# Performance work log

Measured on AMD Instinct MI355X. Metric: run time of the kernel, lower is better.

Reference implementation:

```python
import jax, jax.numpy as jnp
import numpy as np

HIDDEN = 1024
HEADS = 16
HEAD_DIM = HIDDEN // HEADS


def setup_inputs() -> dict:
    key = jax.random.key(0)
    ks = jax.random.split(key, 9)
    B, S = 2, 2048
    std = 1.0 / np.sqrt(HIDDEN)
    inp = {
        'hidden_states': jax.random.normal(ks[0], (B, S, HIDDEN), dtype=jnp.float32),
        'attention_mask': jnp.ones((B, S), dtype=jnp.int32),
        'wq': jax.random.normal(ks[1], (HIDDEN, HIDDEN), dtype=jnp.float32) * std,
        'bq': jnp.zeros((HIDDEN,), dtype=jnp.float32),
        'wk': jax.random.normal(ks[2], (HIDDEN, HIDDEN), dtype=jnp.float32) * std,
        'bk': jnp.zeros((HIDDEN,), dtype=jnp.float32),
        'wv': jax.random.normal(ks[3], (HIDDEN, HIDDEN), dtype=jnp.float32) * std,
        'bv': jnp.zeros((HIDDEN,), dtype=jnp.float32),
        'wo': jax.random.normal(ks[4], (HIDDEN, HIDDEN), dtype=jnp.float32) * std,
        'bo': jnp.zeros((HIDDEN,), dtype=jnp.float32),
    }
    return inp


def reference(hidden_states, attention_mask, wq, bq, wk, bk, wv, bv, wo, bo):
    B, S, H = hidden_states.shape
    def heads(x):  # [B,S,H] -> [B,nh,S,hd]
        return x.reshape(B, S, HEADS, HEAD_DIM).transpose(0, 2, 1, 3)
    q = heads(hidden_states @ wq + bq)
    k = heads(hidden_states @ wk + bk)
    v = heads(hidden_states @ wv + bv)
    scores = jnp.einsum('bhqd,bhkd->bhqk', q, k) / np.sqrt(HEAD_DIM).astype(np.float32)
    causal = jnp.tril(jnp.ones((S, S), dtype=bool))  # True = keep
    keep = causal[None, None] & (attention_mask[:, None, None, :] != 0)
    scores = jnp.where(keep, scores, -jnp.inf)
    probs = jax.nn.softmax(scores, axis=-1)
    out = jnp.einsum('bhqk,bhkd->bhqd', probs, v)  # [B,nh,S,hd]
    out = out.transpose(0, 2, 1, 3).reshape(B, S, H)
    return out @ wo + bo
```

## Files before the change

kernel.cpp:

```cpp
#include <hip/hip_runtime.h>

#define HID   1024
#define SLEN  2048
#define NHEAD 16
#define HDIM  64
#define SC2L  0.18033688f

typedef unsigned short u16;
typedef _Float16 f16;
using bf16x8 = __attribute__((ext_vector_type(8))) short;
using f16x4  = __attribute__((ext_vector_type(4))) f16;
using f32x4  = __attribute__((ext_vector_type(4))) float;

typedef __attribute__((address_space(1))) void gvoid;
typedef __attribute__((address_space(3))) void lvoid;

__device__ __forceinline__ u16 f2bf(float f) {
  union { float f; unsigned u; } v; v.f = f;
  unsigned u = v.u;
  return (u16)((u + 0x7fffu + ((u >> 16) & 1u)) >> 16);
}

__device__ __forceinline__ void async_ld16(const u16* g, u16* l) {
  __builtin_amdgcn_global_load_lds((gvoid*)g, (lvoid*)l, 16, 0, 0);
}

__global__ __launch_bounds__(256) void prep_kernel(const float* __restrict__ x,
                                                   const float* __restrict__ wq,
                                                   const float* __restrict__ wk,
                                                   const float* __restrict__ wv,
                                                   const float* __restrict__ wo,
                                                   u16* __restrict__ xb,
                                                   u16* __restrict__ wt) {
  const int tid = threadIdx.x;
  if (blockIdx.z == 4) {
    const int bid = blockIdx.y * 32 + blockIdx.x;
#pragma unroll
    for (int it = 0; it < 4; ++it) {
      const int i = bid * 1024 + it * 256 + tid;
      float4 v = ((const float4*)x)[i];
      ushort4 o;
      o.x = f2bf(v.x); o.y = f2bf(v.y); o.z = f2bf(v.z); o.w = f2bf(v.w);
      ((ushort4*)xb)[i] = o;
    }
    return;
  }
  const float* src = (blockIdx.z == 0) ? wq : (blockIdx.z == 1) ? wk
                   : (blockIdx.z == 2) ? wv : wo;
  u16* dst = wt + (size_t)blockIdx.z * (HID * HID);
  __shared__ float tile[32][33];
  const int n0 = blockIdx.x * 32, k0 = blockIdx.y * 32;
  const int xx = tid & 31, yy = tid >> 5;
  for (int i = yy; i < 32; i += 8)
    tile[i][xx] = src[(size_t)(k0 + i) * HID + n0 + xx];
  __syncthreads();
  for (int i = yy; i < 32; i += 8)
    dst[(size_t)(n0 + i) * HID + k0 + xx] = f2bf(tile[xx][i]);
}

__global__ __launch_bounds__(256) void gemm_qkv_kernel(const u16* __restrict__ A,
                                                       const u16* __restrict__ Bt,
                                                       const float* __restrict__ bq,
                                                       const float* __restrict__ bk,
                                                       const float* __restrict__ bv,
                                                       u16* __restrict__ Qb,
                                                       u16* __restrict__ Kb,
                                                       u16* __restrict__ VTf) {
  __shared__ u16 smem[8192];
  u16* sA = smem;
  u16* sB = smem + 4096;
  const int tid  = threadIdx.x;
  const int wave = tid >> 6, lane = tid & 63;
  const int quad = lane >> 4, l16 = lane & 15;
  const int n0g = blockIdx.x * 128;
  const int region = blockIdx.x >> 3;
  const int colbase = (blockIdx.x & 7) * 128;
  const int m0 = blockIdx.y * 128;
  const int wm = (wave & 1) * 64, wn = (wave >> 1) * 64;

  f32x4 acc[4][4] = {};
  const int srow = lane >> 2;
  const int scol = (lane & 3) * 8;

  for (int kt = 0; kt < HID; kt += 32) {
    __syncthreads();
    for (int c = wave; c < 8; c += 4) {
      async_ld16(A  + (size_t)(m0  + c * 16 + srow) * HID + kt + scol, &sA[c * 512]);
      async_ld16(Bt + (size_t)(n0g + c * 16 + srow) * HID + kt + scol, &sB[c * 512]);
    }
    __syncthreads();

    bf16x8 af[4], bfr[4];
#pragma unroll
    for (int t = 0; t < 4; ++t) {
      af[t]  = *(const bf16x8*)&sA[(wm + t * 16 + l16) * 32 + quad * 8];
      bfr[t] = *(const bf16x8*)&sB[(wn + t * 16 + l16) * 32 + quad * 8];
    }
#pragma unroll
    for (int mt = 0; mt < 4; ++mt)
#pragma unroll
      for (int nt = 0; nt < 4; ++nt)
        acc[mt][nt] = __builtin_amdgcn_mfma_f32_16x16x32_bf16(af[mt], bfr[nt],
                                                              acc[mt][nt], 0, 0, 0);
  }

  const float* bias = (region == 0) ? bq : (region == 1) ? bk : bv;
  float bvv[4];
#pragma unroll
  for (int nt = 0; nt < 4; ++nt) bvv[nt] = bias[colbase + wn + nt * 16 + l16];

  if (region == 2) {
    const int bb = m0 >> 11;
    const int m0loc = m0 & 2047;
    const int h0 = colbase >> 6;
    u16* T = smem;
#pragma unroll
    for (int h2 = 0; h2 < 2; ++h2) {
      __syncthreads();
      if ((wave >> 1) == h2) {
#pragma unroll
        for (int mt = 0; mt < 4; ++mt)
#pragma unroll
          for (int nt = 0; nt < 4; ++nt)
#pragma unroll
            for (int r = 0; r < 4; ++r) {
              const int sl = (wave & 1) * 64 + mt * 16 + quad * 4 + r;
              const int dl = nt * 16 + l16;
              union { f16 h; u16 u; } cv;
              cv.h = (f16)(acc[mt][nt][r] + bvv[nt]);
              T[dl * 128 + (((sl >> 3) ^ l16) * 8) + (sl & 7)] = cv.u;
            }
      }
      __syncthreads();
      const int d = tid >> 2, sg = (tid & 3) * 4;
      u16* drow = VTf + (size_t)((bb * NHEAD + h0 + h2) * HDIM + d) * SLEN + m0loc;
#pragma unroll
      for (int cc = 0; cc < 4; ++cc) {
        const int cl = sg + cc;
        const int ph = cl ^ (d & 15);
        *(bf16x8*)(drow + cl * 8) = *(const bf16x8*)&T[d * 128 + ph * 8];
      }
    }
    return;
  }

  u16* C = (region == 0) ? Qb : Kb;
#pragma unroll
  for (int mt = 0; mt < 4; ++mt)
#pragma unroll
    for (int r = 0; r < 4; ++r) {
      const int row = m0 + wm + mt * 16 + quad * 4 + r;
#pragma unroll
      for (int nt = 0; nt < 4; ++nt) {
        const int col = colbase + wn + nt * 16 + l16;
        C[(size_t)row * HID + col] = f2bf(acc[mt][nt][r] + bvv[nt]);
      }
    }
}

__global__ __launch_bounds__(256) void gemm_o_kernel(const u16* __restrict__ A,
                                                     const u16* __restrict__ Bt,
                                                     const float* __restrict__ bias,
                                                     float* __restrict__ Cf) {
  __shared__ u16 sA[64 * 32];
  __shared__ u16 sB[128 * 32];
  const int tid  = threadIdx.x;
  const int wave = tid >> 6, lane = tid & 63;
  const int quad = lane >> 4, l16 = lane & 15;
  const int n0 = blockIdx.x * 128;
  const int m0 = blockIdx.y * 64;
  const int wn = wave * 32;

  f32x4 acc[4][2] = {};
  const int srow = lane >> 2;
  const int scol = (lane & 3) * 8;

  for (int kt = 0; kt < HID; kt += 32) {
    __syncthreads();
    for (int c = wave; c < 12; c += 4) {
      if (c < 4) async_ld16(A  + (size_t)(m0 + c * 16 + srow) * HID + kt + scol, &sA[c * 512]);
      else       async_ld16(Bt + (size_t)(n0 + (c - 4) * 16 + srow) * HID + kt + scol,
                            &sB[(c - 4) * 512]);
    }
    __syncthreads();

    bf16x8 af[4], bfr[2];
#pragma unroll
    for (int t = 0; t < 4; ++t)
      af[t] = *(const bf16x8*)&sA[(t * 16 + l16) * 32 + quad * 8];
#pragma unroll
    for (int t = 0; t < 2; ++t)
      bfr[t] = *(const bf16x8*)&sB[(wn + t * 16 + l16) * 32 + quad * 8];
#pragma unroll
    for (int mt = 0; mt < 4; ++mt)
#pragma unroll
      for (int nt = 0; nt < 2; ++nt)
        acc[mt][nt] = __builtin_amdgcn_mfma_f32_16x16x32_bf16(af[mt], bfr[nt],
                                                              acc[mt][nt], 0, 0, 0);
  }

  float bvv[2];
#pragma unroll
  for (int nt = 0; nt < 2; ++nt) bvv[nt] = bias[n0 + wn + nt * 16 + l16];
#pragma unroll
  for (int mt = 0; mt < 4; ++mt)
#pragma unroll
    for (int r = 0; r < 4; ++r) {
      const int row = m0 + mt * 16 + quad * 4 + r;
#pragma unroll
      for (int nt = 0; nt < 2; ++nt)
        Cf[(size_t)row * HID + n0 + wn + nt * 16 + l16] = acc[mt][nt][r] + bvv[nt];
    }
}

__global__ __launch_bounds__(256, 2) void flash_attn_kernel(const u16* __restrict__ Q,
                                                            const u16* __restrict__ K,
                                                            const u16* __restrict__ VT,
                                                            const int* __restrict__ mask,
                                                            u16* __restrict__ O) {
  const int xb = blockIdx.x, h = blockIdx.y, b = blockIdx.z;
  const int tid  = threadIdx.x;
  const int wave = tid >> 6, lane = tid & 63;
  const int quad = lane >> 4, l16 = lane & 15;

  __shared__ alignas(16) char smraw[35840];
  u16*   Ks  = (u16*)smraw;
  u16*   Vt  = (u16*)(smraw + 16384);
  float* Ob0 = (float*)smraw;
  float* Ob1 = (float*)(smraw + 16896);
  float* lb  = (float*)(smraw + 33792);

  const u16* Kh  = K  + (size_t)b * SLEN * HID + h * HDIM;
  const u16* Vth = VT + (size_t)((b * NHEAD + h) * HDIM) * SLEN;

  const int srow8 = lane >> 3;
  const int gch   = (lane & 7) ^ srow8;
  const int rx    = l16 & 7;

  for (int phase = 0; phase < 2; ++phase) {
    const int qt = phase ? (31 - xb) : xb;
    const int q0 = qt * 64;

    bf16x8 qb[4][2];
#pragma unroll
    for (int nt = 0; nt < 4; ++nt) {
      const u16* qp = Q + (size_t)(b * SLEN + q0 + nt * 16 + l16) * HID + h * HDIM + quad * 8;
      qb[nt][0] = *(const bf16x8*)qp;
      qb[nt][1] = *(const bf16x8*)(qp + 32);
    }

    f32x4 oacc[4][4] = {};
    float l_part[4] = {0.f, 0.f, 0.f, 0.f};

    {
      const int r0 = wave * 16 + srow8;
      async_ld16(Kh  + (size_t)r0 * HID + gch * 8,        Ks + wave * 1024);
      async_ld16(Kh  + (size_t)(r0 + 8) * HID + gch * 8,  Ks + wave * 1024 + 512);
      async_ld16(Vth + (size_t)r0 * SLEN + gch * 8,       Vt + wave * 1024);
      async_ld16(Vth + (size_t)(r0 + 8) * SLEN + gch * 8, Vt + wave * 1024 + 512);
    }
    __syncthreads();

    for (int j = 0; j <= qt; ++j) {
      const int buf = j & 1;
      u16* KsB = Ks + buf * 4096;
      u16* VtB = Vt + buf * 4096;

      if (j < qt) {
        const int nb = (buf ^ 1) * 4096;
        const int jn = (j + 1) * 64;
        const int r0 = wave * 16 + srow8;
        async_ld16(Kh  + (size_t)(jn + r0) * HID + gch * 8,       Ks + nb + wave * 1024);
        async_ld16(Kh  + (size_t)(jn + r0 + 8) * HID + gch * 8,   Ks + nb + wave * 1024 + 512);
        async_ld16(Vth + (size_t)r0 * SLEN + jn + gch * 8,        Vt + nb + wave * 1024);
        async_ld16(Vth + (size_t)(r0 + 8) * SLEN + jn + gch * 8,  Vt + nb + wave * 1024 + 512);
      }

      const int4 mi = *(const int4*)(mask + b * SLEN + j * 64 + wave * 16 + quad * 4);
      float map[4];
      map[0] = mi.x ? 0.f : -1e30f;  map[1] = mi.y ? 0.f : -1e30f;
      map[2] = mi.z ? 0.f : -1e30f;  map[3] = mi.w ? 0.f : -1e30f;

      const u16* kp = KsB + (wave * 16 + l16) * 64;
      const int ph0 = quad ^ rx;
      const bf16x8 ka0 = *(const bf16x8*)(kp + ph0 * 8);
      const bf16x8 ka1 = *(const bf16x8*)(kp + (ph0 ^ 4) * 8);

      float p[4][4];
#pragma unroll
      for (int nt = 0; nt < 4; ++nt) {
        f32x4 z = {0.f, 0.f, 0.f, 0.f};
        z = __builtin_amdgcn_mfma_f32_16x16x32_bf16(ka0, qb[nt][0], z, 0, 0, 0);
        z = __builtin_amdgcn_mfma_f32_16x16x32_bf16(ka1, qb[nt][1], z, 0, 0, 0);
#pragma unroll
        for (int r = 0; r < 4; ++r)
          p[nt][r] = exp2f(fmaf(z[r], SC2L, map[r]));
      }
      if (j == qt) {
#pragma unroll
        for (int nt = 0; nt < 4; ++nt)
#pragma unroll
          for (int r = 0; r < 4; ++r)
            if (wave * 16 + quad * 4 + r > nt * 16 + l16) p[nt][r] = 0.f;
      }

      f16x4 pb[4];
#pragma unroll
      for (int nt = 0; nt < 4; ++nt) {
        l_part[nt] += (p[nt][0] + p[nt][1]) + (p[nt][2] + p[nt][3]);
        pb[nt][0] = (f16)p[nt][0]; pb[nt][1] = (f16)p[nt][1];
        pb[nt][2] = (f16)p[nt][2]; pb[nt][3] = (f16)p[nt][3];
      }

      const int phv = (wave * 2 + (quad >> 1)) ^ rx;
      const int vsub = phv * 8 + (quad & 1) * 4;
#pragma unroll
      for (int dt = 0; dt < 4; ++dt) {
        const f16x4 va = *(const f16x4*)(VtB + (dt * 16 + l16) * 64 + vsub);
#pragma unroll
        for (int nt = 0; nt < 4; ++nt)
          oacc[dt][nt] = __builtin_amdgcn_mfma_f32_16x16x16f16(va, pb[nt], oacc[dt][nt], 0, 0, 0);
      }
      __syncthreads();
    }

#pragma unroll
    for (int nt = 0; nt < 4; ++nt) {
      l_part[nt] += __shfl_xor(l_part[nt], 16);
      l_part[nt] += __shfl_xor(l_part[nt], 32);
    }
    if (quad == 0)
#pragma unroll
      for (int nt = 0; nt < 4; ++nt) lb[wave * 64 + nt * 16 + l16] = l_part[nt];

    if ((wave & 1) == 0) {
      float* ob = (wave == 0) ? Ob0 : Ob1;
#pragma unroll
      for (int dt = 0; dt < 4; ++dt)
#pragma unroll
        for (int nt = 0; nt < 4; ++nt)
#pragma unroll
          for (int r = 0; r < 4; ++r)
            ob[(dt * 16 + quad * 4 + r) * 66 + nt * 16 + l16] = oacc[dt][nt][r];
    }
    __syncthreads();
    if (wave & 1) {
      float* ob = (wave == 1) ? Ob0 : Ob1;
#pragma unroll
      for (int dt = 0; dt < 4; ++dt)
#pragma unroll
        for (int nt = 0; nt < 4; ++nt)
#pragma unroll
          for (int r = 0; r < 4; ++r)
            ob[(dt * 16 + quad * 4 + r) * 66 + nt * 16 + l16] += oacc[dt][nt][r];
    }
    __syncthreads();

    {
      const int q  = tid >> 2;
      const int dc = tid & 3;
      const float l = lb[q] + lb[64 + q] + lb[128 + q] + lb[192 + q];
      const float inv = 1.f / l;
      u16 ob[16];
#pragma unroll
      for (int e = 0; e < 16; ++e) {
        const int d = dc * 16 + e;
        ob[e] = f2bf((Ob0[d * 66 + q] + Ob1[d * 66 + q]) * inv);
      }
      u16* op = O + (size_t)(b * SLEN + q0 + q) * HID + h * HDIM + dc * 16;
      *(bf16x8*)op       = *(bf16x8*)&ob[0];
      *(bf16x8*)(op + 8) = *(bf16x8*)&ob[8];
    }
    __syncthreads();
  }
}

extern "C" void kernel_launch(void* const* d_in, const int* in_sizes, int n_in,
                              void* d_out, int out_size, void* d_ws, size_t ws_size,
                              hipStream_t stream) {
  const float* x    = (const float*)d_in[0];
  const int*   mask = (const int*)d_in[1];
  const float* wq   = (const float*)d_in[2];
  const float* bq   = (const float*)d_in[3];
  const float* wk   = (const float*)d_in[4];
  const float* bk   = (const float*)d_in[5];
  const float* wv   = (const float*)d_in[6];
  const float* bv   = (const float*)d_in[7];
  const float* wo   = (const float*)d_in[8];
  const float* bo   = (const float*)d_in[9];
  float* out = (float*)d_out;

  char* ws = (char*)d_ws;
  u16* XBF = (u16*)(ws);
  u16* WT  = (u16*)(ws + (8u  << 20));
  u16* QBF = (u16*)(ws + (16u << 20));
  u16* KBF = (u16*)(ws + (24u << 20));
  u16* VTF = (u16*)(ws + (32u << 20));
  u16* ATT = (u16*)(ws);

  prep_kernel<<<dim3(32, 32, 5), 256, 0, stream>>>(x, wq, wk, wv, wo, XBF, WT);
  gemm_qkv_kernel<<<dim3(24, 32), 256, 0, stream>>>(XBF, WT, bq, bk, bv, QBF, KBF, VTF);
  flash_attn_kernel<<<dim3(16, NHEAD, 2), 256, 0, stream>>>(QBF, KBF, VTF, mask, ATT);
  gemm_o_kernel<<<dim3(8, 64), 256, 0, stream>>>(ATT, WT + (3u << 20), bo, out);
}
```

Measured before the change: 205.2 us.

## Double the attention key tile to 128 rows and pack P with cvt_pkrtz

The flash attention loop now processes 128 keys per iteration instead of 64. Each wave handles two 16-row sub-tiles, so the number of loop iterations and __syncthreads barriers per query tile is halved. The K/V shared buffers double to about 66KB with a new XOR swizzle for the 128-wide V rows, and the causal mask is applied by global index on the last tile. The probabilities are converted to fp16 with packed round-toward-zero conversions. The larger LDS footprint may reduce occupancy relative to launch_bounds(256,2), and the last tile now does extra work on keys that are masked out.

```diff
diff --git a/kernel.cpp b/kernel.cpp
--- a/kernel.cpp
+++ b/kernel.cpp
@@ -9,6 +9,8 @@
 typedef unsigned short u16;
 typedef _Float16 f16;
 using bf16x8 = __attribute__((ext_vector_type(8))) short;
+using h16x2  = __attribute__((ext_vector_type(2))) __fp16;
+using h16x4  = __attribute__((ext_vector_type(4))) __fp16;
 using f16x4  = __attribute__((ext_vector_type(4))) f16;
 using f32x4  = __attribute__((ext_vector_type(4))) float;
 
@@ -223,23 +225,24 @@
   const int wave = tid >> 6, lane = tid & 63;
   const int quad = lane >> 4, l16 = lane & 15;
 
-  __shared__ alignas(16) char smraw[35840];
-  u16*   Ks  = (u16*)smraw;
-  u16*   Vt  = (u16*)(smraw + 16384);
+  __shared__ alignas(16) char smraw[66560];
+  u16*   Ks = (u16*)smraw;
+  u16*   Vt = (u16*)(smraw + 32768);
+  float* lb = (float*)(smraw + 65536);
   float* Ob0 = (float*)smraw;
   float* Ob1 = (float*)(smraw + 16896);
-  float* lb  = (float*)(smraw + 33792);
 
   const u16* Kh  = K  + (size_t)b * SLEN * HID + h * HDIM;
   const u16* Vth = VT + (size_t)((b * NHEAD + h) * HDIM) * SLEN;
 
-  const int srow8 = lane >> 3;
-  const int gch   = (lane & 7) ^ srow8;
-  const int rx    = l16 & 7;
+  const int kr8 = lane >> 3, kc = lane & 7;
+  const int kgch = kc ^ (kr8 & 7);
+  const int vdl = lane >> 4, vc = lane & 15;
 
   for (int phase = 0; phase < 2; ++phase) {
     const int qt = phase ? (31 - xb) : xb;
     const int q0 = qt * 64;
+    const int jn = (qt >> 1) + 1;
 
     bf16x8 qb[4][2];
 #pragma unroll
@@ -252,74 +255,93 @@
     f32x4 oacc[4][4] = {};
     float l_part[4] = {0.f, 0.f, 0.f, 0.f};
 
-    {
-      const int r0 = wave * 16 + srow8;
-      async_ld16(Kh  + (size_t)r0 * HID + gch * 8,        Ks + wave * 1024);
-      async_ld16(Kh  + (size_t)(r0 + 8) * HID + gch * 8,  Ks + wave * 1024 + 512);
-      async_ld16(Vth + (size_t)r0 * SLEN + gch * 8,       Vt + wave * 1024);
-      async_ld16(Vth + (size_t)(r0 + 8) * SLEN + gch * 8, Vt + wave * 1024 + 512);
-    }
-    __syncthreads();
-
-    for (int j = 0; j <= qt; ++j) {
+#pragma unroll
+    for (int a = 0; a < 4; ++a) {
+      async_ld16(Kh + (size_t)(wave * 32 + a * 8 + kr8) * HID + kgch * 8,
+                 Ks + (wave * 32 + a * 8) * 64);
+      const int d = wave * 16 + a * 4 + vdl;
+      async_ld16(Vth + (size_t)d * SLEN + (vc ^ (d & 15)) * 8,
+                 Vt + (wave * 16 + a * 4) * 128);
+    }
+    __syncthreads();
+
+    for (int j = 0; j < jn; ++j) {
       const int buf = j & 1;
-      u16* KsB = Ks + buf * 4096;
-      u16* VtB = Vt + buf * 4096;
-
-      if (j < qt) {
-        const int nb = (buf ^ 1) * 4096;
-        const int jn = (j + 1) * 64;
-        const int r0 = wave * 16 + srow8;
-        async_ld16(Kh  + (size_t)(jn + r0) * HID + gch * 8,       Ks + nb + wave * 1024);
-        async_ld16(Kh  + (size_t)(jn + r0 + 8) * HID + gch * 8,   Ks + nb + wave * 1024 + 512);
-        async_ld16(Vth + (size_t)r0 * SLEN + jn + gch * 8,        Vt + nb + wave * 1024);
-        async_ld16(Vth + (size_t)(r0 + 8) * SLEN + jn + gch * 8,  Vt + nb + wave * 1024 + 512);
-      }
-
-      const int4 mi = *(const int4*)(mask + b * SLEN + j * 64 + wave * 16 + quad * 4);
-      float map[4];
-      map[0] = mi.x ? 0.f : -1e30f;  map[1] = mi.y ? 0.f : -1e30f;
-      map[2] = mi.z ? 0.f : -1e30f;  map[3] = mi.w ? 0.f : -1e30f;
-
-      const u16* kp = KsB + (wave * 16 + l16) * 64;
-      const int ph0 = quad ^ rx;
-      const bf16x8 ka0 = *(const bf16x8*)(kp + ph0 * 8);
-      const bf16x8 ka1 = *(const bf16x8*)(kp + (ph0 ^ 4) * 8);
-
-      float p[4][4];
-#pragma unroll
-      for (int nt = 0; nt < 4; ++nt) {
-        f32x4 z = {0.f, 0.f, 0.f, 0.f};
-        z = __builtin_amdgcn_mfma_f32_16x16x32_bf16(ka0, qb[nt][0], z, 0, 0, 0);
-        z = __builtin_amdgcn_mfma_f32_16x16x32_bf16(ka1, qb[nt][1], z, 0, 0, 0);
-#pragma unroll
-        for (int r = 0; r < 4; ++r)
-          p[nt][r] = exp2f(fmaf(z[r], SC2L, map[r]));
-      }
-      if (j == qt) {
-#pragma unroll
-        for (int nt = 0; nt < 4; ++nt)
+      u16* KsB = Ks + buf * 8192;
+      u16* VtB = Vt + buf * 8192;
+
+      if (j + 1 < jn) {
+        u16* Kd = Ks + (buf ^ 1) * 8192;
+        u16* Vd = Vt + (buf ^ 1) * 8192;
+        const int kb = (j + 1) * 128;
+#pragma unroll
+        for (int a = 0; a < 4; ++a) {
+          async_ld16(Kh + (size_t)(kb + wave * 32 + a * 8 + kr8) * HID + kgch * 8,
+                     Kd + (wave * 32 + a * 8) * 64);
+          const int d = wave * 16 + a * 4 + vdl;
+          async_ld16(Vth + (size_t)d * SLEN + kb + (vc ^ (d & 15)) * 8,
+                     Vd + (wave * 16 + a * 4) * 128);
+        }
+      }
+
+      float p[2][4][4];
+#pragma unroll
+      for (int sub = 0; sub < 2; ++sub) {
+        const int krow = wave * 32 + sub * 16 + l16;
+        const u16* kp = KsB + krow * 64;
+        const int ph0 = quad ^ (l16 & 7);
+        const bf16x8 ka0 = *(const bf16x8*)(kp + ph0 * 8);
+        const bf16x8 ka1 = *(const bf16x8*)(kp + (ph0 ^ 4) * 8);
+        const int4 mi = *(const int4*)(mask + b * SLEN + j * 128 + wave * 32 + sub * 16 + quad * 4);
+        float map[4];
+        map[0] = mi.x ? 0.f : -1e30f;  map[1] = mi.y ? 0.f : -1e30f;
+        map[2] = mi.z ? 0.f : -1e30f;  map[3] = mi.w ? 0.f : -1e30f;
+#pragma unroll
+        for (int nt = 0; nt < 4; ++nt) {
+          f32x4 z = {0.f, 0.f, 0.f, 0.f};
+          z = __builtin_amdgcn_mfma_f32_16x16x32_bf16(ka0, qb[nt][0], z, 0, 0, 0);
+          z = __builtin_amdgcn_mfma_f32_16x16x32_bf16(ka1, qb[nt][1], z, 0, 0, 0);
 #pragma unroll
           for (int r = 0; r < 4; ++r)
-            if (wave * 16 + quad * 4 + r > nt * 16 + l16) p[nt][r] = 0.f;
-      }
-
-      f16x4 pb[4];
-#pragma unroll
-      for (int nt = 0; nt < 4; ++nt) {
-        l_part[nt] += (p[nt][0] + p[nt][1]) + (p[nt][2] + p[nt][3]);
-        pb[nt][0] = (f16)p[nt][0]; pb[nt][1] = (f16)p[nt][1];
-        pb[nt][2] = (f16)p[nt][2]; pb[nt][3] = (f16)p[nt][3];
-      }
-
-      const int phv = (wave * 2 + (quad >> 1)) ^ rx;
-      const int vsub = phv * 8 + (quad & 1) * 4;
+            p[sub][nt][r] = exp2f(fmaf(z[r], SC2L, map[r]));
+        }
+      }
+      if (j == jn - 1) {
+#pragma unroll
+        for (int sub = 0; sub < 2; ++sub)
+#pragma unroll
+          for (int nt = 0; nt < 4; ++nt)
+#pragma unroll
+            for (int r = 0; r < 4; ++r) {
+              const int kg = j * 128 + wave * 32 + sub * 16 + quad * 4 + r;
+              if (kg > q0 + nt * 16 + l16) p[sub][nt][r] = 0.f;
+            }
+      }
+
+      f16x4 pb[2][4];
+#pragma unroll
+      for (int sub = 0; sub < 2; ++sub)
+#pragma unroll
+        for (int nt = 0; nt < 4; ++nt) {
+          l_part[nt] += (p[sub][nt][0] + p[sub][nt][1]) + (p[sub][nt][2] + p[sub][nt][3]);
+          const h16x2 lo = __builtin_amdgcn_cvt_pkrtz(p[sub][nt][0], p[sub][nt][1]);
+          const h16x2 hi = __builtin_amdgcn_cvt_pkrtz(p[sub][nt][2], p[sub][nt][3]);
+          const h16x4 packed = __builtin_shufflevector(lo, hi, 0, 1, 2, 3);
+          pb[sub][nt] = __builtin_bit_cast(f16x4, packed);
+        }
+
 #pragma unroll
       for (int dt = 0; dt < 4; ++dt) {
-        const f16x4 va = *(const f16x4*)(VtB + (dt * 16 + l16) * 64 + vsub);
-#pragma unroll
-        for (int nt = 0; nt < 4; ++nt)
-          oacc[dt][nt] = __builtin_amdgcn_mfma_f32_16x16x16f16(va, pb[nt], oacc[dt][nt], 0, 0, 0);
+        const int d = dt * 16 + l16;
+#pragma unroll
+        for (int sub = 0; sub < 2; ++sub) {
+          const int ph = (wave * 4 + sub * 2 + (quad >> 1)) ^ l16;
+          const f16x4 va = *(const f16x4*)(VtB + d * 128 + ph * 8 + (quad & 1) * 4);
+#pragma unroll
+          for (int nt = 0; nt < 4; ++nt)
+            oacc[dt][nt] = __builtin_amdgcn_mfma_f32_16x16x16f16(va, pb[sub][nt],
+                                                                 oacc[dt][nt], 0, 0, 0);
+        }
       }
       __syncthreads();
     }
```

Result: no change. 206.1 us (+0.4%).

## Use one q-tile per block with triple-buffered K/V and bitmask mask

Applied to the files above, without the earlier changes.

The flash attention kernel now launches one block per 64-row query tile instead of pairing tiles in two phases, and staggers tile order by head and batch to spread causal work. K/V loads move from double to triple buffering, with custom barriers that wait only on the older loads. The attention mask is packed into a shared-memory bitmask once per block and applied with a select after exp2 instead of an additive bias. Probability packing uses cvt_pkrtz, and launch bounds request three blocks per CU. This trades the paired-tile load balancing for more blocks and deeper prefetch, and the larger shared-memory footprint may limit occupancy.

```diff
diff --git a/kernel.cpp b/kernel.cpp
--- a/kernel.cpp
+++ b/kernel.cpp
@@ -7,8 +7,11 @@
 #define SC2L  0.18033688f
 
 typedef unsigned short u16;
+typedef unsigned int u32;
 typedef _Float16 f16;
 using bf16x8 = __attribute__((ext_vector_type(8))) short;
+using h16x2  = __attribute__((ext_vector_type(2))) __fp16;
+using h16x4  = __attribute__((ext_vector_type(4))) __fp16;
 using f16x4  = __attribute__((ext_vector_type(4))) f16;
 using f32x4  = __attribute__((ext_vector_type(4))) float;
 
@@ -23,6 +26,13 @@
 
 __device__ __forceinline__ void async_ld16(const u16* g, u16* l) {
   __builtin_amdgcn_global_load_lds((gvoid*)g, (lvoid*)l, 16, 0, 0);
+}
+
+__device__ __forceinline__ void barrier_keep4() {
+  asm volatile("s_waitcnt vmcnt(4)\ns_barrier" ::: "memory");
+}
+__device__ __forceinline__ void barrier_keep0() {
+  asm volatile("s_waitcnt vmcnt(0)\ns_barrier" ::: "memory");
 }
 
 __global__ __launch_bounds__(256) void prep_kernel(const float* __restrict__ x,
@@ -213,165 +223,179 @@
     }
 }
 
-__global__ __launch_bounds__(256, 2) void flash_attn_kernel(const u16* __restrict__ Q,
+__global__ __launch_bounds__(256, 3) void flash_attn_kernel(const u16* __restrict__ Q,
                                                             const u16* __restrict__ K,
                                                             const u16* __restrict__ VT,
                                                             const int* __restrict__ mask,
                                                             u16* __restrict__ O) {
-  const int xb = blockIdx.x, h = blockIdx.y, b = blockIdx.z;
+  const int h = blockIdx.y, b = blockIdx.z;
+  const int qt = (blockIdx.x + 2 * h + b) & 31;
   const int tid  = threadIdx.x;
   const int wave = tid >> 6, lane = tid & 63;
   const int quad = lane >> 4, l16 = lane & 15;
-
-  __shared__ alignas(16) char smraw[35840];
-  u16*   Ks  = (u16*)smraw;
-  u16*   Vt  = (u16*)(smraw + 16384);
-  float* Ob0 = (float*)smraw;
-  float* Ob1 = (float*)(smraw + 16896);
-  float* lb  = (float*)(smraw + 33792);
+  const int q0 = qt * 64;
+  const int jmax = qt + 1;
+
+  __shared__ alignas(16) char smraw[50688];
+  u16*   mb32 = (u16*)(smraw + 49152);
+  float* lb   = (float*)(smraw + 49664);
+  float* Ob0  = (float*)smraw;
+  float* Ob1  = (float*)(smraw + 16896);
 
   const u16* Kh  = K  + (size_t)b * SLEN * HID + h * HDIM;
   const u16* Vth = VT + (size_t)((b * NHEAD + h) * HDIM) * SLEN;
 
-  const int srow8 = lane >> 3;
-  const int gch   = (lane & 7) ^ srow8;
-  const int rx    = l16 & 7;
-
-  for (int phase = 0; phase < 2; ++phase) {
-    const int qt = phase ? (31 - xb) : xb;
-    const int q0 = qt * 64;
-
-    bf16x8 qb[4][2];
+  {
+    const int4 m0i = *(const int4*)(mask + b * SLEN + tid * 8);
+    const int4 m1i = *(const int4*)(mask + b * SLEN + tid * 8 + 4);
+    unsigned byte = (m0i.x ? 1u : 0u) | (m0i.y ? 2u : 0u) | (m0i.z ? 4u : 0u) |
+                    (m0i.w ? 8u : 0u) | (m1i.x ? 16u : 0u) | (m1i.y ? 32u : 0u) |
+                    (m1i.z ? 64u : 0u) | (m1i.w ? 128u : 0u);
+    ((unsigned char*)mb32)[tid] = (unsigned char)byte;
+  }
+
+  bf16x8 qb[4][2];
+#pragma unroll
+  for (int nt = 0; nt < 4; ++nt) {
+    const u16* qp = Q + (size_t)(b * SLEN + q0 + nt * 16 + l16) * HID + h * HDIM + quad * 8;
+    qb[nt][0] = *(const bf16x8*)qp;
+    qb[nt][1] = *(const bf16x8*)(qp + 32);
+  }
+  __syncthreads();
+
+  f32x4 oacc[4][4] = {};
+  float l_part[4] = {0.f, 0.f, 0.f, 0.f};
+
+  const int kr8 = lane >> 3, kc = lane & 7;
+  const int gch = kc ^ kr8;
+
+#define STAGE(J, IDX)                                                            \
+  {                                                                              \
+    u16* Kp = (u16*)smraw + (IDX) * 8192;                                        \
+    u16* Vp = Kp + 4096;                                                         \
+    const int kb_ = (J) * 64;                                                    \
+    async_ld16(Kh + (size_t)(kb_ + wave * 16 + kr8) * HID + gch * 8,             \
+               Kp + (wave * 16) * 64);                                           \
+    async_ld16(Kh + (size_t)(kb_ + wave * 16 + 8 + kr8) * HID + gch * 8,         \
+               Kp + (wave * 16 + 8) * 64);                                       \
+    async_ld16(Vth + (size_t)(wave * 16 + kr8) * SLEN + kb_ + gch * 8,           \
+               Vp + (wave * 16) * 64);                                           \
+    async_ld16(Vth + (size_t)(wave * 16 + 8 + kr8) * SLEN + kb_ + gch * 8,       \
+               Vp + (wave * 16 + 8) * 64);                                       \
+  }
+
+  STAGE(0, 0);
+  if (jmax > 1) { STAGE(1, 1); barrier_keep4(); }
+  else          { barrier_keep0(); }
+
+  const int rx = l16 & 7;
+  const int ph0 = quad ^ rx;
+  const int vslot = (wave * 2 + (quad >> 1)) ^ rx;
+  const int vsub = vslot * 8 + (quad & 1) * 4;
+
+  for (int j = 0; j < jmax; ++j) {
+    u16* KsB = (u16*)smraw + (j % 3) * 8192;
+    u16* VtB = KsB + 4096;
+    const bool pf = (j + 2 < jmax);
+    if (pf) STAGE(j + 2, (j + 2) % 3);
+
+    const unsigned mword = ((const u32*)mb32)[j * 2 + (wave >> 1)];
+    const unsigned mb4 = (mword >> (((wave & 1) * 16) + quad * 4)) & 0xFu;
+
+    const u16* kp = KsB + (wave * 16 + l16) * 64;
+    const bf16x8 ka0 = *(const bf16x8*)(kp + ph0 * 8);
+    const bf16x8 ka1 = *(const bf16x8*)(kp + (ph0 ^ 4) * 8);
+
+    float p[4][4];
 #pragma unroll
     for (int nt = 0; nt < 4; ++nt) {
-      const u16* qp = Q + (size_t)(b * SLEN + q0 + nt * 16 + l16) * HID + h * HDIM + quad * 8;
-      qb[nt][0] = *(const bf16x8*)qp;
-      qb[nt][1] = *(const bf16x8*)(qp + 32);
-    }
-
-    f32x4 oacc[4][4] = {};
-    float l_part[4] = {0.f, 0.f, 0.f, 0.f};
-
-    {
-      const int r0 = wave * 16 + srow8;
-      async_ld16(Kh  + (size_t)r0 * HID + gch * 8,        Ks + wave * 1024);
-      async_ld16(Kh  + (size_t)(r0 + 8) * HID + gch * 8,  Ks + wave * 1024 + 512);
-      async_ld16(Vth + (size_t)r0 * SLEN + gch * 8,       Vt + wave * 1024);
-      async_ld16(Vth + (size_t)(r0 + 8) * SLEN + gch * 8, Vt + wave * 1024 + 512);
-    }
-    __syncthreads();
-
-    for (int j = 0; j <= qt; ++j) {
-      const int buf = j & 1;
-      u16* KsB = Ks + buf * 4096;
-      u16* VtB = Vt + buf * 4096;
-
-      if (j < qt) {
-        const int nb = (buf ^ 1) * 4096;
-        const int jn = (j + 1) * 64;
-        const int r0 = wave * 16 + srow8;
-        async_ld16(Kh  + (size_t)(jn + r0) * HID + gch * 8,       Ks + nb + wave * 1024);
-        async_ld16(Kh  + (size_t)(jn + r0 + 8) * HID + gch * 8,   Ks + nb + wave * 1024 + 512);
-        async_ld16(Vth + (size_t)r0 * SLEN + jn + gch * 8,        Vt + nb + wave * 1024);
-        async_ld16(Vth + (size_t)(r0 + 8) * SLEN + jn + gch * 8,  Vt + nb + wave * 1024 + 512);
+      f32x4 z = {0.f, 0.f, 0.f, 0.f};
+      z = __builtin_amdgcn_mfma_f32_16x16x32_bf16(ka0, qb[nt][0], z, 0, 0, 0);
+      z = __builtin_amdgcn_mfma_f32_16x16x32_bf16(ka1, qb[nt][1], z, 0, 0, 0);
+#pragma unroll
+      for (int r = 0; r < 4; ++r) {
+        float pv = exp2f(z[r] * SC2L);
+        pv = (mb4 & (1u << r)) ? pv : 0.f;
+        p[nt][r] = pv;
       }
-
-      const int4 mi = *(const int4*)(mask + b * SLEN + j * 64 + wave * 16 + quad * 4);
-      float map[4];
-      map[0] = mi.x ? 0.f : -1e30f;  map[1] = mi.y ? 0.f : -1e30f;
-      map[2] = mi.z ? 0.f : -1e30f;  map[3] = mi.w ? 0.f : -1e30f;
-
-      const u16* kp = KsB + (wave * 16 + l16) * 64;
-      const int ph0 = quad ^ rx;
-      const bf16x8 ka0 = *(const bf16x8*)(kp + ph0 * 8);
-      const bf16x8 ka1 = *(const bf16x8*)(kp + (ph0 ^ 4) * 8);
-
-      float p[4][4];
-#pragma unroll
-      for (int nt = 0; nt < 4; ++nt) {
-        f32x4 z = {0.f, 0.f, 0.f, 0.f};
-        z = __builtin_amdgcn_mfma_f32_16x16x32_bf16(ka0, qb[nt][0], z, 0, 0, 0);
-        z = __builtin_amdgcn_mfma_f32_16x16x32_bf16(ka1, qb[nt][1], z, 0, 0, 0);
+    }
+    if (j == jmax - 1) {
+#pragma unroll
+      for (int nt = 0; nt < 4; ++nt)
 #pragma unroll
         for (int r = 0; r < 4; ++r)
-          p[nt][r] = exp2f(fmaf(z[r], SC2L, map[r]));
-      }
-      if (j == qt) {
-#pragma unroll
-        for (int nt = 0; nt < 4; ++nt)
-#pragma unroll
-          for (int r = 0; r < 4; ++r)
-            if (wave * 16 + quad * 4 + r > nt * 16 + l16) p[nt][r] = 0.f;
-      }
-
-      f16x4 pb[4];
-#pragma unroll
-      for (int nt = 0; nt < 4; ++nt) {
-        l_part[nt] += (p[nt][0] + p[nt][1]) + (p[nt][2] + p[nt][3]);
-        pb[nt][0] = (f16)p[nt][0]; pb[nt][1] = (f16)p[nt][1];
-        pb[nt][2] = (f16)p[nt][2]; pb[nt][3] = (f16)p[nt][3];
-      }
-
-      const int phv = (wave * 2 + (quad >> 1)) ^ rx;
-      const int vsub = phv * 8 + (quad & 1) * 4;
-#pragma unroll
-      for (int dt = 0; dt < 4; ++dt) {
-        const f16x4 va = *(const f16x4*)(VtB + (dt * 16 + l16) * 64 + vsub);
-#pragma unroll
-        for (int nt = 0; nt < 4; ++nt)
-          oacc[dt][nt] = __builtin_amdgcn_mfma_f32_16x16x16f16(va, pb[nt], oacc[dt][nt], 0, 0, 0);
-      }
-      __syncthreads();
-    }
-
+          if (wave * 16 + quad * 4 + r > nt * 16 + l16) p[nt][r] = 0.f;
+    }
+
+    f16x4 pb[4];
 #pragma unroll
     for (int nt = 0; nt < 4; ++nt) {
-      l_part[nt] += __shfl_xor(l_part[nt], 16);
-      l_part[nt] += __shfl_xor(l_part[nt], 32);
-    }
-    if (quad == 0)
-#pragma unroll
-      for (int nt = 0; nt < 4; ++nt) lb[wave * 64 + nt * 16 + l16] = l_part[nt];
-
-    if ((wave & 1) == 0) {
-      float* ob = (wave == 0) ? Ob0 : Ob1;
-#pragma unroll
-      for (int dt = 0; dt < 4; ++dt)
-#pragma unroll
-        for (int nt = 0; nt < 4; ++nt)
-#pragma unroll
-          for (int r = 0; r < 4; ++r)
-            ob[(dt * 16 + quad * 4 + r) * 66 + nt * 16 + l16] = oacc[dt][nt][r];
-    }
-    __syncthreads();
-    if (wave & 1) {
-      float* ob = (wave == 1) ? Ob0 : Ob1;
-#pragma unroll
-      for (int dt = 0; dt < 4; ++dt)
-#pragma unroll
-        for (int nt = 0; nt < 4; ++nt)
-#pragma unroll
-          for (int r = 0; r < 4; ++r)
-            ob[(dt * 16 + quad * 4 + r) * 66 + nt * 16 + l16] += oacc[dt][nt][r];
-    }
-    __syncthreads();
-
-    {
-      const int q  = tid >> 2;
-      const int dc = tid & 3;
-      const float l = lb[q] + lb[64 + q] + lb[128 + q] + lb[192 + q];
-      const float inv = 1.f / l;
-      u16 ob[16];
-#pragma unroll
-      for (int e = 0; e < 16; ++e) {
-        const int d = dc * 16 + e;
-        ob[e] = f2bf((Ob0[d * 66 + q] + Ob1[d * 66 + q]) * inv);
-      }
-      u16* op = O + (size_t)(b * SLEN + q0 + q) * HID + h * HDIM + dc * 16;
-      *(bf16x8*)op       = *(bf16x8*)&ob[0];
-      *(bf16x8*)(op + 8) = *(bf16x8*)&ob[8];
-    }
-    __syncthreads();
+      l_part[nt] += (p[nt][0] + p[nt][1]) + (p[nt][2] + p[nt][3]);
+      const h16x2 lo = __builtin_amdgcn_cvt_pkrtz(p[nt][0], p[nt][1]);
+      const h16x2 hi = __builtin_amdgcn_cvt_pkrtz(p[nt][2], p[nt][3]);
+      const h16x4 packed = __builtin_shufflevector(lo, hi, 0, 1, 2, 3);
+      pb[nt] = __builtin_bit_cast(f16x4, packed);
+    }
+
+#pragma unroll
+    for (int dt = 0; dt < 4; ++dt) {
+      const f16x4 va = *(const f16x4*)(VtB + (dt * 16 + l16) * 64 + vsub);
+#pragma unroll
+      for (int nt = 0; nt < 4; ++nt)
+        oacc[dt][nt] = __builtin_amdgcn_mfma_f32_16x16x16f16(va, pb[nt], oacc[dt][nt], 0, 0, 0);
+    }
+
+    if (pf) barrier_keep4();
+    else    barrier_keep0();
+  }
+#undef STAGE
+
+#pragma unroll
+  for (int nt = 0; nt < 4; ++nt) {
+    l_part[nt] += __shfl_xor(l_part[nt], 16);
+    l_part[nt] += __shfl_xor(l_part[nt], 32);
+  }
+  if (quad == 0)
+#pragma unroll
+    for (int nt = 0; nt < 4; ++nt) lb[wave * 64 + nt * 16 + l16] = l_part[nt];
+
+  if ((wave & 1) == 0) {
+    float* ob = (wave == 0) ? Ob0 : Ob1;
+#pragma unroll
+    for (int dt = 0; dt < 4; ++dt)
+#pragma unroll
+      for (int nt = 0; nt < 4; ++nt)
+#pragma unroll
+        for (int r = 0; r < 4; ++r)
+          ob[(dt * 16 + quad * 4 + r) * 66 + nt * 16 + l16] = oacc[dt][nt][r];
+  }
+  __syncthreads();
+  if (wave & 1) {
+    float* ob = (wave == 1) ? Ob0 : Ob1;
+#pragma unroll
+    for (int dt = 0; dt < 4; ++dt)
+#pragma unroll
+      for (int nt = 0; nt < 4; ++nt)
+#pragma unroll
+        for (int r = 0; r < 4; ++r)
+          ob[(dt * 16 + quad * 4 + r) * 66 + nt * 16 + l16] += oacc[dt][nt][r];
+  }
+  __syncthreads();
+
+  {
+    const int q  = tid >> 2;
+    const int dc = tid & 3;
+    const float l = lb[q] + lb[64 + q] + lb[128 + q] + lb[192 + q];
+    const float inv = 1.f / l;
+    u16 ob[16];
+#pragma unroll
+    for (int e = 0; e < 16; ++e) {
+      const int d = dc * 16 + e;
+      ob[e] = f2bf((Ob0[d * 66 + q] + Ob1[d * 66 + q]) * inv);
+    }
+    u16* op = O + (size_t)(b * SLEN + q0 + q) * HID + h * HDIM + dc * 16;
+    *(bf16x8*)op       = *(bf16x8*)&ob[0];
+    *(bf16x8*)(op + 8) = *(bf16x8*)&ob[8];
   }
 }
 
@@ -400,6 +424,6 @@
 
   prep_kernel<<<dim3(32, 32, 5), 256, 0, stream>>>(x, wq, wk, wv, wo, XBF, WT);
   gemm_qkv_kernel<<<dim3(24, 32), 256, 0, stream>>>(XBF, WT, bq, bk, bv, QBF, KBF, VTF);
-  flash_attn_kernel<<<dim3(16, NHEAD, 2), 256, 0, stream>>>(QBF, KBF, VTF, mask, ATT);
+  flash_attn_kernel<<<dim3(32, NHEAD, 2), 256, 0, stream>>>(QBF, KBF, VTF, mask, ATT);
   gemm_o_kernel<<<dim3(8, 64), 256, 0, stream>>>(ATT, WT + (3u << 20), bo, out);
 }
```

Result: slower. 210.6 us (+2.6%).

## Double K-step per sync in GEMMs with XOR-swizzled LDS and packed f16 convert

Applied to the files above, without the earlier changes.

Both projection GEMMs now stage a 64-wide K slice per iteration instead of 32, halving the number of barrier pairs, and use an XOR swizzle on the LDS chunk layout to avoid bank conflicts on the fragment reads. LDS footprint per block doubles, which may reduce occupancy. In attention, the probability-to-f16 conversion uses packed round-toward-zero conversions instead of four scalar casts, slightly changing rounding.

```diff
diff --git a/kernel.cpp b/kernel.cpp
--- a/kernel.cpp
+++ b/kernel.cpp
@@ -7,8 +7,11 @@
 #define SC2L  0.18033688f
 
 typedef unsigned short u16;
+typedef unsigned int u32;
 typedef _Float16 f16;
 using bf16x8 = __attribute__((ext_vector_type(8))) short;
+using h16x2  = __attribute__((ext_vector_type(2))) __fp16;
+using h16x4  = __attribute__((ext_vector_type(4))) __fp16;
 using f16x4  = __attribute__((ext_vector_type(4))) f16;
 using f32x4  = __attribute__((ext_vector_type(4))) float;
 
@@ -66,9 +69,9 @@
                                                        u16* __restrict__ Qb,
                                                        u16* __restrict__ Kb,
                                                        u16* __restrict__ VTf) {
-  __shared__ u16 smem[8192];
+  __shared__ u16 smem[16384];
   u16* sA = smem;
-  u16* sB = smem + 4096;
+  u16* sB = smem + 8192;
   const int tid  = threadIdx.x;
   const int wave = tid >> 6, lane = tid & 63;
   const int quad = lane >> 4, l16 = lane & 15;
@@ -79,22 +82,34 @@
   const int wm = (wave & 1) * 64, wn = (wave >> 1) * 64;
 
   f32x4 acc[4][4] = {};
-  const int srow = lane >> 2;
-  const int scol = (lane & 3) * 8;
-
-  for (int kt = 0; kt < HID; kt += 32) {
-    __syncthreads();
-    for (int c = wave; c < 8; c += 4) {
-      async_ld16(A  + (size_t)(m0  + c * 16 + srow) * HID + kt + scol, &sA[c * 512]);
-      async_ld16(Bt + (size_t)(n0g + c * 16 + srow) * HID + kt + scol, &sB[c * 512]);
+  const int sr8 = lane >> 3;
+  const int gch = (lane & 7) ^ sr8;
+  const int px  = quad ^ (l16 & 7);
+
+  for (int kt = 0; kt < HID; kt += 64) {
+    __syncthreads();
+    for (int c = wave; c < 16; c += 4) {
+      async_ld16(A  + (size_t)(m0  + c * 8 + sr8) * HID + kt + gch * 8, &sA[c * 512]);
+      async_ld16(Bt + (size_t)(n0g + c * 8 + sr8) * HID + kt + gch * 8, &sB[c * 512]);
     }
     __syncthreads();
 
     bf16x8 af[4], bfr[4];
 #pragma unroll
     for (int t = 0; t < 4; ++t) {
-      af[t]  = *(const bf16x8*)&sA[(wm + t * 16 + l16) * 32 + quad * 8];
-      bfr[t] = *(const bf16x8*)&sB[(wn + t * 16 + l16) * 32 + quad * 8];
+      af[t]  = *(const bf16x8*)&sA[(wm + t * 16 + l16) * 64 + px * 8];
+      bfr[t] = *(const bf16x8*)&sB[(wn + t * 16 + l16) * 64 + px * 8];
+    }
+#pragma unroll
+    for (int mt = 0; mt < 4; ++mt)
+#pragma unroll
+      for (int nt = 0; nt < 4; ++nt)
+        acc[mt][nt] = __builtin_amdgcn_mfma_f32_16x16x32_bf16(af[mt], bfr[nt],
+                                                              acc[mt][nt], 0, 0, 0);
+#pragma unroll
+    for (int t = 0; t < 4; ++t) {
+      af[t]  = *(const bf16x8*)&sA[(wm + t * 16 + l16) * 64 + (px ^ 4) * 8];
+      bfr[t] = *(const bf16x8*)&sB[(wn + t * 16 + l16) * 64 + (px ^ 4) * 8];
     }
 #pragma unroll
     for (int mt = 0; mt < 4; ++mt)
@@ -162,8 +177,9 @@
                                                      const u16* __restrict__ Bt,
                                                      const float* __restrict__ bias,
                                                      float* __restrict__ Cf) {
-  __shared__ u16 sA[64 * 32];
-  __shared__ u16 sB[128 * 32];
+  __shared__ u16 smem[12288];
+  u16* sA = smem;
+  u16* sB = smem + 4096;
   const int tid  = threadIdx.x;
   const int wave = tid >> 6, lane = tid & 63;
   const int quad = lane >> 4, l16 = lane & 15;
@@ -172,25 +188,39 @@
   const int wn = wave * 32;
 
   f32x4 acc[4][2] = {};
-  const int srow = lane >> 2;
-  const int scol = (lane & 3) * 8;
-
-  for (int kt = 0; kt < HID; kt += 32) {
-    __syncthreads();
-    for (int c = wave; c < 12; c += 4) {
-      if (c < 4) async_ld16(A  + (size_t)(m0 + c * 16 + srow) * HID + kt + scol, &sA[c * 512]);
-      else       async_ld16(Bt + (size_t)(n0 + (c - 4) * 16 + srow) * HID + kt + scol,
-                            &sB[(c - 4) * 512]);
+  const int sr8 = lane >> 3;
+  const int gch = (lane & 7) ^ sr8;
+  const int px  = quad ^ (l16 & 7);
+
+  for (int kt = 0; kt < HID; kt += 64) {
+    __syncthreads();
+    for (int c = wave; c < 24; c += 4) {
+      if (c < 8) async_ld16(A  + (size_t)(m0 + c * 8 + sr8) * HID + kt + gch * 8,
+                            &sA[c * 512]);
+      else       async_ld16(Bt + (size_t)(n0 + (c - 8) * 8 + sr8) * HID + kt + gch * 8,
+                            &sB[(c - 8) * 512]);
     }
     __syncthreads();
 
     bf16x8 af[4], bfr[2];
 #pragma unroll
     for (int t = 0; t < 4; ++t)
-      af[t] = *(const bf16x8*)&sA[(t * 16 + l16) * 32 + quad * 8];
+      af[t] = *(const bf16x8*)&sA[(t * 16 + l16) * 64 + px * 8];
 #pragma unroll
     for (int t = 0; t < 2; ++t)
-      bfr[t] = *(const bf16x8*)&sB[(wn + t * 16 + l16) * 32 + quad * 8];
+      bfr[t] = *(const bf16x8*)&sB[(wn + t * 16 + l16) * 64 + px * 8];
+#pragma unroll
+    for (int mt = 0; mt < 4; ++mt)
+#pragma unroll
+      for (int nt = 0; nt < 2; ++nt)
+        acc[mt][nt] = __builtin_amdgcn_mfma_f32_16x16x32_bf16(af[mt], bfr[nt],
+                                                              acc[mt][nt], 0, 0, 0);
+#pragma unroll
+    for (int t = 0; t < 4; ++t)
+      af[t] = *(const bf16x8*)&sA[(t * 16 + l16) * 64 + (px ^ 4) * 8];
+#pragma unroll
+    for (int t = 0; t < 2; ++t)
+      bfr[t] = *(const bf16x8*)&sB[(wn + t * 16 + l16) * 64 + (px ^ 4) * 8];
 #pragma unroll
     for (int mt = 0; mt < 4; ++mt)
 #pragma unroll
@@ -308,8 +338,10 @@
 #pragma unroll
       for (int nt = 0; nt < 4; ++nt) {
         l_part[nt] += (p[nt][0] + p[nt][1]) + (p[nt][2] + p[nt][3]);
-        pb[nt][0] = (f16)p[nt][0]; pb[nt][1] = (f16)p[nt][1];
-        pb[nt][2] = (f16)p[nt][2]; pb[nt][3] = (f16)p[nt][3];
+        const h16x2 lo = __builtin_amdgcn_cvt_pkrtz(p[nt][0], p[nt][1]);
+        const h16x2 hi = __builtin_amdgcn_cvt_pkrtz(p[nt][2], p[nt][3]);
+        const h16x4 packed = __builtin_shufflevector(lo, hi, 0, 1, 2, 3);
+        pb[nt] = __builtin_bit_cast(f16x4, packed);
       }
 
       const int phv = (wave * 2 + (quad >> 1)) ^ rx;
```

Result: slower. 209.6 us (+2.1%).
